# Optimization experiments

Hardware: AMD Instinct MI355X
Metric: run time of the kernel (lower is better)

## Reference

```python
import jax, jax.numpy as jnp
import numpy as np

DIM = 2048
DIM_SEQ = 2048
DIM_OUT = DIM // 2
LN_EPS = 1e-5


def setup_inputs() -> dict:
    key = jax.random.key(0)
    k1, k2 = jax.random.split(key)
    x = jax.random.normal(k1, (8, DIM_SEQ, DIM), dtype=jnp.float32)
    init_eps = 0.001 / DIM_SEQ
    # Conv1d(dim_seq, dim_seq, 1) weight -> [seq, seq] seq-mixing matrix
    proj_w = jax.random.uniform(k2, (DIM_SEQ, DIM_SEQ), minval=-init_eps, maxval=init_eps, dtype=jnp.float32)
    proj_b = jnp.ones((DIM_SEQ,), dtype=jnp.float32)
    ln_scale = jnp.ones((DIM_OUT,), dtype=jnp.float32)
    ln_bias = jnp.zeros((DIM_OUT,), dtype=jnp.float32)
    return {"x": x, "proj_w": proj_w, "proj_b": proj_b, "ln_scale": ln_scale, "ln_bias": ln_bias}


def reference(x, proj_w, proj_b, ln_scale, ln_bias):
    # chunk into residual and gate halves along feature dim
    res, gate = jnp.split(x, 2, axis=-1)  # each [b, s, d/2]
    # LayerNorm over last dim of gate
    mu = jnp.mean(gate, axis=-1, keepdims=True)
    var = jnp.mean(jnp.square(gate - mu), axis=-1, keepdims=True)
    gate = (gate - mu) * jax.lax.rsqrt(var + LN_EPS) * ln_scale + ln_bias
    # Conv1d kernel=1 over seq axis == seq-mixing matmul: [s,t] x [b,t,d] -> [b,s,d]
    gate = jnp.einsum('st,btd->bsd', proj_w, gate) + proj_b[None, :, None]
    # act = Identity; gated residual multiply
    return gate * res
```

## Files before the change

kernel.cpp:

```cpp
#include <hip/hip_runtime.h>

typedef __attribute__((ext_vector_type(8))) short short8;
typedef __attribute__((ext_vector_type(4))) float floatx4;

__device__ __forceinline__ unsigned short f2bf(float f) {
    unsigned int u = __builtin_bit_cast(unsigned int, f);
    u += 0x7fffu + ((u >> 16) & 1u);
    return (unsigned short)(u >> 16);
}

__device__ __forceinline__ void async16(unsigned short* lds, const unsigned short* g) {
    __builtin_amdgcn_global_load_lds(
        (__attribute__((address_space(1))) void*)(g),
        (__attribute__((address_space(3))) void*)(lds),
        16, 0, 0);
}

#define DIM      2048
#define DSEQ     2048
#define DOUT     1024
#define NBATCH   8

__global__ __launch_bounds__(256) void cast_w_kernel(const float* __restrict__ w,
                                                     unsigned short* __restrict__ o) {
    int i = (blockIdx.x * 256 + threadIdx.x) * 4;
    float4 v = *(const float4*)(w + i);
    unsigned int lo = (unsigned int)f2bf(v.x) | ((unsigned int)f2bf(v.y) << 16);
    unsigned int hi = (unsigned int)f2bf(v.z) | ((unsigned int)f2bf(v.w) << 16);
    *(uint2*)(o + i) = make_uint2(lo, hi);
}

__global__ __launch_bounds__(256) void ln_t_kernel(const float* __restrict__ X,
                                                   const float* __restrict__ lns,
                                                   const float* __restrict__ lnb,
                                                   unsigned short* __restrict__ Gt) {
    const int tid  = threadIdx.x;
    const int wave = tid >> 6;
    const int lane = tid & 63;
    const int t0   = blockIdx.x * 32;
    const int b    = blockIdx.y;

    __shared__ unsigned short lt[32][1028];

    #pragma unroll
    for (int i = 0; i < 8; ++i) {
        const int r = wave * 8 + i;
        const float* xr = X + ((size_t)(b * DSEQ + t0 + r)) * DIM + DOUT;
        float4 v[4];
        float s = 0.f, ss = 0.f;
        #pragma unroll
        for (int c = 0; c < 4; ++c) {
            v[c] = *(const float4*)(xr + c * 256 + lane * 4);
            s  += v[c].x + v[c].y + v[c].z + v[c].w;
            ss += v[c].x * v[c].x + v[c].y * v[c].y + v[c].z * v[c].z + v[c].w * v[c].w;
        }
        #pragma unroll
        for (int off = 32; off > 0; off >>= 1) {
            s  += __shfl_xor(s,  off, 64);
            ss += __shfl_xor(ss, off, 64);
        }
        const float mu  = s * (1.f / 1024.f);
        const float var = ss * (1.f / 1024.f) - mu * mu;
        const float inv = rsqrtf(var + 1e-5f);
        #pragma unroll
        for (int c = 0; c < 4; ++c) {
            const int d = c * 256 + lane * 4;
            float4 sc = *(const float4*)(lns + d);
            float4 bi = *(const float4*)(lnb + d);
            float y0 = (v[c].x - mu) * inv * sc.x + bi.x;
            float y1 = (v[c].y - mu) * inv * sc.y + bi.y;
            float y2 = (v[c].z - mu) * inv * sc.z + bi.z;
            float y3 = (v[c].w - mu) * inv * sc.w + bi.w;
            unsigned int lo = (unsigned int)f2bf(y0) | ((unsigned int)f2bf(y1) << 16);
            unsigned int hi = (unsigned int)f2bf(y2) | ((unsigned int)f2bf(y3) << 16);
            *(uint2*)&lt[r][d] = make_uint2(lo, hi);
        }
    }
    __syncthreads();

    #pragma unroll
    for (int it = 0; it < 4; ++it) {
        const int d = it * 256 + tid;
        unsigned int u[16];
        #pragma unroll
        for (int j = 0; j < 16; ++j)
            u[j] = (unsigned int)lt[2 * j][d] | ((unsigned int)lt[2 * j + 1][d] << 16);
        uint4* dst = (uint4*)(Gt + ((size_t)(b * DOUT + d)) * DSEQ + t0);
        dst[0] = make_uint4(u[0],  u[1],  u[2],  u[3]);
        dst[1] = make_uint4(u[4],  u[5],  u[6],  u[7]);
        dst[2] = make_uint4(u[8],  u[9],  u[10], u[11]);
        dst[3] = make_uint4(u[12], u[13], u[14], u[15]);
    }
}

#define BM 128
#define BN 128
#define BK 32

__global__ __launch_bounds__(256) void gemm_sgu(const unsigned short* __restrict__ Wb,
                                                const unsigned short* __restrict__ Gt,
                                                const float* __restrict__ X,
                                                const float* __restrict__ Pb,
                                                float* __restrict__ Out) {
    const int K   = DSEQ;
    const int tid = threadIdx.x;
    const int s0  = blockIdx.x * BM;
    const int d0  = blockIdx.y * BN;
    const int b   = blockIdx.z;

    __shared__ unsigned short As[BM * BK];
    __shared__ unsigned short Bs[BN * BK];

    const int wave = tid >> 6;
    const int lane = tid & 63;
    const int wr   = wave >> 1;
    const int wc   = wave & 1;
    const int ln15 = lane & 15;
    const int q    = lane >> 4;

    const int row = tid >> 2;
    const int c8  = (tid & 3) * 8;

    floatx4 acc[4][4] = {};

    const unsigned short* aG = Wb + (size_t)s0 * K;
    const unsigned short* bG = Gt + ((size_t)(b * DOUT + d0)) * K;

    for (int k0 = 0; k0 < K; k0 += BK) {
        __syncthreads();
        async16(&As[(size_t)row * BK + c8],        aG + (size_t)row * K        + k0 + c8);
        async16(&As[(size_t)(row + 64) * BK + c8], aG + (size_t)(row + 64) * K + k0 + c8);
        async16(&Bs[(size_t)row * BK + c8],        bG + (size_t)row * K        + k0 + c8);
        async16(&Bs[(size_t)(row + 64) * BK + c8], bG + (size_t)(row + 64) * K + k0 + c8);
        __syncthreads();

        short8 af[4], bf[4];
        #pragma unroll
        for (int i = 0; i < 4; ++i)
            af[i] = *(const short8*)&As[(wr * 64 + i * 16 + ln15) * BK + q * 8];
        #pragma unroll
        for (int i = 0; i < 4; ++i)
            bf[i] = *(const short8*)&Bs[(wc * 64 + i * 16 + ln15) * BK + q * 8];
        #pragma unroll
        for (int i = 0; i < 4; ++i)
            #pragma unroll
            for (int j = 0; j < 4; ++j)
                acc[i][j] = __builtin_amdgcn_mfma_f32_16x16x32_bf16(af[i], bf[j], acc[i][j], 0, 0, 0);
    }

    #pragma unroll
    for (int i = 0; i < 4; ++i) {
        const int srow = s0 + wr * 64 + i * 16 + q * 4;
        #pragma unroll
        for (int j = 0; j < 4; ++j) {
            const int d = d0 + wc * 64 + j * 16 + ln15;
            #pragma unroll
            for (int r = 0; r < 4; ++r) {
                const int s = srow + r;
                const float g = acc[i][j][r] + Pb[s];
                const size_t xi = ((size_t)(b * DSEQ + s)) * DIM + d;
                const size_t oi = ((size_t)(b * DSEQ + s)) * DOUT + d;
                Out[oi] = g * X[xi];
            }
        }
    }
}

extern "C" void kernel_launch(void* const* d_in, const int* in_sizes, int n_in,
                              void* d_out, int out_size, void* d_ws, size_t ws_size,
                              hipStream_t stream) {
    const float* x    = (const float*)d_in[0];
    const float* pw   = (const float*)d_in[1];
    const float* pb   = (const float*)d_in[2];
    const float* lns  = (const float*)d_in[3];
    const float* lnb  = (const float*)d_in[4];
    float* out        = (float*)d_out;

    unsigned short* Wb = (unsigned short*)d_ws;
    unsigned short* Gt = (unsigned short*)((char*)d_ws + (size_t)DSEQ * DSEQ * 2);

    cast_w_kernel<<<dim3((DSEQ * DSEQ) / 1024), dim3(256), 0, stream>>>(pw, Wb);
    ln_t_kernel<<<dim3(DSEQ / 32, NBATCH), dim3(256), 0, stream>>>(x, lns, lnb, Gt);
    gemm_sgu<<<dim3(DSEQ / BM, DOUT / BN, NBATCH), dim3(256), 0, stream>>>(Wb, Gt, x, pb, out);
}
```

Baseline: 324.7 us.

## Block K-panel layout for W and G and double K-step per barrier

The cast and LN kernels now write W and the transposed gate in a K-blocked layout ([kblock][row][32]). This turns each GEMM tile load into a contiguous span, so the async global-to-LDS loads coalesce fully. The GEMM also processes 64 K per iteration, two 32-wide sub-panels, which halves the number of barrier pairs. The cost is double the LDS use per block, and the LDS read pattern with a 32-element row stride may still hit bank conflicts.

```diff
diff --git a/kernel.cpp b/kernel.cpp
--- a/kernel.cpp
+++ b/kernel.cpp
@@ -20,14 +20,18 @@
 #define DSEQ     2048
 #define DOUT     1024
 #define NBATCH   8
+#define NKB      (DSEQ / 32)
 
 __global__ __launch_bounds__(256) void cast_w_kernel(const float* __restrict__ w,
                                                      unsigned short* __restrict__ o) {
     int i = (blockIdx.x * 256 + threadIdx.x) * 4;
+    int s = i >> 11;
+    int t = i & 2047;
     float4 v = *(const float4*)(w + i);
     unsigned int lo = (unsigned int)f2bf(v.x) | ((unsigned int)f2bf(v.y) << 16);
     unsigned int hi = (unsigned int)f2bf(v.z) | ((unsigned int)f2bf(v.w) << 16);
-    *(uint2*)(o + i) = make_uint2(lo, hi);
+    unsigned short* dst = o + (((size_t)(t >> 5)) * DSEQ + s) * 32 + (t & 31);
+    *(uint2*)dst = make_uint2(lo, hi);
 }
 
 __global__ __launch_bounds__(256) void ln_t_kernel(const float* __restrict__ X,
@@ -85,7 +89,7 @@
         #pragma unroll
         for (int j = 0; j < 16; ++j)
             u[j] = (unsigned int)lt[2 * j][d] | ((unsigned int)lt[2 * j + 1][d] << 16);
-        uint4* dst = (uint4*)(Gt + ((size_t)(b * DOUT + d)) * DSEQ + t0);
+        uint4* dst = (uint4*)(Gt + (((size_t)b * NKB + (t0 >> 5)) * DOUT + d) * 32);
         dst[0] = make_uint4(u[0],  u[1],  u[2],  u[3]);
         dst[1] = make_uint4(u[4],  u[5],  u[6],  u[7]);
         dst[2] = make_uint4(u[8],  u[9],  u[10], u[11]);
@@ -95,21 +99,20 @@
 
 #define BM 128
 #define BN 128
-#define BK 32
+#define BK 64
 
-__global__ __launch_bounds__(256) void gemm_sgu(const unsigned short* __restrict__ Wb,
+__global__ __launch_bounds__(256) void gemm_sgu(const unsigned short* __restrict__ Wt,
                                                 const unsigned short* __restrict__ Gt,
                                                 const float* __restrict__ X,
                                                 const float* __restrict__ Pb,
                                                 float* __restrict__ Out) {
-    const int K   = DSEQ;
     const int tid = threadIdx.x;
     const int s0  = blockIdx.x * BM;
     const int d0  = blockIdx.y * BN;
     const int b   = blockIdx.z;
 
-    __shared__ unsigned short As[BM * BK];
-    __shared__ unsigned short Bs[BN * BK];
+    __shared__ unsigned short As[2 * BM * 32];
+    __shared__ unsigned short Bs[2 * BN * 32];
 
     const int wave = tid >> 6;
     const int lane = tid & 63;
@@ -118,34 +121,39 @@
     const int ln15 = lane & 15;
     const int q    = lane >> 4;
 
-    const int row = tid >> 2;
-    const int c8  = (tid & 3) * 8;
-
     floatx4 acc[4][4] = {};
 
-    const unsigned short* aG = Wb + (size_t)s0 * K;
-    const unsigned short* bG = Gt + ((size_t)(b * DOUT + d0)) * K;
+    for (int k0 = 0; k0 < DSEQ; k0 += BK) {
+        const int kb = k0 >> 5;
+        const unsigned short* aG = Wt + ((size_t)kb * DSEQ + s0) * 32;
+        const unsigned short* bG = Gt + (((size_t)b * NKB + kb) * DOUT + d0) * 32;
 
-    for (int k0 = 0; k0 < K; k0 += BK) {
         __syncthreads();
-        async16(&As[(size_t)row * BK + c8],        aG + (size_t)row * K        + k0 + c8);
-        async16(&As[(size_t)(row + 64) * BK + c8], aG + (size_t)(row + 64) * K + k0 + c8);
-        async16(&Bs[(size_t)row * BK + c8],        bG + (size_t)row * K        + k0 + c8);
-        async16(&Bs[(size_t)(row + 64) * BK + c8], bG + (size_t)(row + 64) * K + k0 + c8);
+        #pragma unroll
+        for (int j = 0; j < 2; ++j) {
+            const int ch = tid + j * 256;
+            async16(&As[(size_t)ch * 8],        aG + (size_t)ch * 8);
+            async16(&As[4096 + (size_t)ch * 8], aG + (size_t)DSEQ * 32 + (size_t)ch * 8);
+            async16(&Bs[(size_t)ch * 8],        bG + (size_t)ch * 8);
+            async16(&Bs[4096 + (size_t)ch * 8], bG + (size_t)DOUT * 32 + (size_t)ch * 8);
+        }
         __syncthreads();
 
-        short8 af[4], bf[4];
         #pragma unroll
-        for (int i = 0; i < 4; ++i)
-            af[i] = *(const short8*)&As[(wr * 64 + i * 16 + ln15) * BK + q * 8];
-        #pragma unroll
-        for (int i = 0; i < 4; ++i)
-            bf[i] = *(const short8*)&Bs[(wc * 64 + i * 16 + ln15) * BK + q * 8];
-        #pragma unroll
-        for (int i = 0; i < 4; ++i)
+        for (int u = 0; u < 2; ++u) {
+            short8 af[4], bf[4];
             #pragma unroll
-            for (int j = 0; j < 4; ++j)
-                acc[i][j] = __builtin_amdgcn_mfma_f32_16x16x32_bf16(af[i], bf[j], acc[i][j], 0, 0, 0);
+            for (int i = 0; i < 4; ++i)
+                af[i] = *(const short8*)&As[(u * BM + wr * 64 + i * 16 + ln15) * 32 + q * 8];
+            #pragma unroll
+            for (int i = 0; i < 4; ++i)
+                bf[i] = *(const short8*)&Bs[(u * BN + wc * 64 + i * 16 + ln15) * 32 + q * 8];
+            #pragma unroll
+            for (int i = 0; i < 4; ++i)
+                #pragma unroll
+                for (int j = 0; j < 4; ++j)
+                    acc[i][j] = __builtin_amdgcn_mfma_f32_16x16x32_bf16(af[i], bf[j], acc[i][j], 0, 0, 0);
+        }
     }
 
     #pragma unroll
@@ -176,10 +184,10 @@
     const float* lnb  = (const float*)d_in[4];
     float* out        = (float*)d_out;
 
-    unsigned short* Wb = (unsigned short*)d_ws;
+    unsigned short* Wt = (unsigned short*)d_ws;
     unsigned short* Gt = (unsigned short*)((char*)d_ws + (size_t)DSEQ * DSEQ * 2);
 
-    cast_w_kernel<<<dim3((DSEQ * DSEQ) / 1024), dim3(256), 0, stream>>>(pw, Wb);
+    cast_w_kernel<<<dim3((DSEQ * DSEQ) / 1024), dim3(256), 0, stream>>>(pw, Wt);
     ln_t_kernel<<<dim3(DSEQ / 32, NBATCH), dim3(256), 0, stream>>>(x, lns, lnb, Gt);
-    gemm_sgu<<<dim3(DSEQ / BM, DOUT / BN, NBATCH), dim3(256), 0, stream>>>(Wb, Gt, x, pb, out);
+    gemm_sgu<<<dim3(DSEQ / BM, DOUT / BN, NBATCH), dim3(256), 0, stream>>>(Wt, Gt, x, pb, out);
 }
```

Result: faster. 313.6 us (-3.4%).
